# Kernel optimization log

Measured on AMD Instinct MI355X. Metric: run time of the kernel, lower is better.

## Reference

```python
import jax, jax.numpy as jnp
import numpy as np


def setup_inputs() -> dict:
    key = jax.random.key(0)
    k1, k2 = jax.random.split(key)
    B, N, M, D = 8, 4096, 4096, 128
    points1 = jax.random.normal(k1, (B, N, D), dtype=jnp.float32)
    points2 = jax.random.normal(k2, (B, M, D), dtype=jnp.float32)
    return {"points1": points1, "points2": points2}


def reference(points1, points2):
    # sum((x[:, :, None] - y[:, None, :])**2, -1), expressed as a GEMM).
    sq1 = jnp.sum(points1 * points1, axis=-1)              # [B, N]
    sq2 = jnp.sum(points2 * points2, axis=-1)              # [B, M]
    cross = jnp.einsum("bnd,bmd->bnm", points1, points2)   # [B, N, M]
    dist_matrix = sq1[:, :, None] + sq2[:, None, :] - 2.0 * cross
    min_dist1 = jnp.min(dist_matrix, axis=2)               # [B, N]
    min_dist2 = jnp.min(dist_matrix, axis=1)               # [B, M]
    return jnp.mean(min_dist1) + jnp.mean(min_dist2)
```

## Files before the change

### kernel.cpp

```cpp
#include <hip/hip_runtime.h>
#include <hip/hip_bf16.h>


#define BATCH 8
#define NPTS 4096
#define DIM 128

using bf16x8 = __attribute__((ext_vector_type(8))) short;
using f32x4  = __attribute__((ext_vector_type(4))) float;

__global__ void prep_kernel(const float* __restrict__ p1,
                            const float* __restrict__ p2,
                            __hip_bfloat16* __restrict__ b1,
                            __hip_bfloat16* __restrict__ b2,
                            float* __restrict__ s1,
                            float* __restrict__ s2) {
    const int arr = blockIdx.y;
    const float* src = arr ? p2 : p1;
    __hip_bfloat16* dst = arr ? b2 : b1;
    float* sq = arr ? s2 : s1;
    const float scale = arr ? 1.0f : -2.0f;

    const int wid = threadIdx.x >> 6;
    const int l   = threadIdx.x & 63;
    const int p   = blockIdx.x * 4 + wid;
    const float2 v = *reinterpret_cast<const float2*>(src + (size_t)p * DIM + l * 2);
    float s = v.x * v.x + v.y * v.y;
    __hip_bfloat162 h = __float22bfloat162_rn(make_float2(v.x * scale, v.y * scale));
    *reinterpret_cast<__hip_bfloat162*>(dst + (size_t)p * DIM + l * 2) = h;
    #pragma unroll
    for (int off = 1; off < 64; off <<= 1) s += __shfl_xor(s, off);
    if (l == 0) sq[p] = s;
}

__device__ __forceinline__ void stage16(const __hip_bfloat16* g, void* lds) {
    __builtin_amdgcn_global_load_lds(
        (const __attribute__((address_space(1))) void*)g,
        (__attribute__((address_space(3))) void*)lds, 16, 0, 0);
}

__global__ void __launch_bounds__(256, 2)
chamfer_tile_kernel(const __hip_bfloat16* __restrict__ bf1,
                    const __hip_bfloat16* __restrict__ bf2,
                    const float* __restrict__ sq1,
                    const float* __restrict__ sq2,
                    float* __restrict__ min1p,
                    float* __restrict__ min2p) {
    const int nt = blockIdx.x;
    const int mh = blockIdx.y;
    const int b  = blockIdx.z;
    const int tid = threadIdx.x;
    const int wid = tid >> 6;
    const int l   = tid & 63;
    const int l15 = l & 15;
    const int lhi = l >> 4;

    __shared__ __align__(16) unsigned char btile[2][128 * 256];

    const __hip_bfloat16* bf1b = bf1 + (size_t)b * NPTS * DIM;
    const __hip_bfloat16* bf2b = bf2 + (size_t)b * NPTS * DIM;
    const float* sq2b = sq2 + b * NPTS;

    const int n0 = nt * 128 + wid * 32;

    bf16x8 afrag[2][4];
    #pragma unroll
    for (int rt = 0; rt < 2; ++rt)
        #pragma unroll
        for (int ks = 0; ks < 4; ++ks)
            afrag[rt][ks] = *reinterpret_cast<const bf16x8*>(
                bf1b + (n0 + rt * 16 + l15) * DIM + ks * 32 + lhi * 8);

    float sq1v[2][4];
    #pragma unroll
    for (int rt = 0; rt < 2; ++rt)
        #pragma unroll
        for (int j = 0; j < 4; ++j)
            sq1v[rt][j] = sq1[b * NPTS + n0 + rt * 16 + lhi * 4 + j];

    float rmin[2][4];
    #pragma unroll
    for (int rt = 0; rt < 2; ++rt)
        #pragma unroll
        for (int j = 0; j < 4; ++j) rmin[rt][j] = 3.4e38f;

    auto STAGE = [&](int buf, int m0) {
        #pragma unroll
        for (int j = 0; j < 8; ++j) {
            const int c   = j * 256 + wid * 64 + l;
            const int row = c >> 4;
            const int q   = c & 15;
            const __hip_bfloat16* src =
                bf2b + (size_t)(m0 + row) * DIM + (q ^ (row & 7)) * 8;
            stage16(src, &btile[buf][(j * 256 + wid * 64) * 16]);
        }
    };

    int cur = 0;
    STAGE(0, mh * 1024);
    __syncthreads();

    for (int mt = 0; mt < 8; ++mt) {
        const int m0 = mh * 1024 + mt * 128;
        if (mt < 7) STAGE(cur ^ 1, m0 + 128);

        f32x4 acc[2][8];
        #pragma unroll
        for (int rt = 0; rt < 2; ++rt)
            #pragma unroll
            for (int ct = 0; ct < 8; ++ct) acc[rt][ct] = f32x4{0.f, 0.f, 0.f, 0.f};

        #pragma unroll
        for (int ks = 0; ks < 4; ++ks) {
            #pragma unroll
            for (int ct = 0; ct < 8; ++ct) {
                const int brow = ct * 16 + l15;
                const int kbyte = ks * 64 + lhi * 16;
                bf16x8 bfrag = *reinterpret_cast<const bf16x8*>(
                    &btile[cur][brow * 256 + (kbyte ^ ((brow & 7) << 4))]);
                #pragma unroll
                for (int rt = 0; rt < 2; ++rt)
                    acc[rt][ct] = __builtin_amdgcn_mfma_f32_16x16x32_bf16(
                        afrag[rt][ks], bfrag, acc[rt][ct], 0, 0, 0);
            }
        }

        float s2v[8];
        #pragma unroll
        for (int ct = 0; ct < 8; ++ct) s2v[ct] = sq2b[m0 + ct * 16 + l15];

        #pragma unroll
        for (int rt = 0; rt < 2; ++rt)
            #pragma unroll
            for (int j = 0; j < 4; ++j) {
                float r = rmin[rt][j];
                #pragma unroll
                for (int cp = 0; cp < 4; ++cp) {
                    const float t0 = acc[rt][2 * cp][j]     + s2v[2 * cp];
                    const float t1 = acc[rt][2 * cp + 1][j] + s2v[2 * cp + 1];
                    r = fminf(r, fminf(t0, t1));
                }
                rmin[rt][j] = r;
            }

        float cmin[8];
        #pragma unroll
        for (int ct = 0; ct < 8; ++ct) {
            float c = 3.4e38f;
            #pragma unroll
            for (int rt = 0; rt < 2; ++rt)
                #pragma unroll
                for (int jp = 0; jp < 2; ++jp) {
                    const float u0 = sq1v[rt][2 * jp]     + acc[rt][ct][2 * jp];
                    const float u1 = sq1v[rt][2 * jp + 1] + acc[rt][ct][2 * jp + 1];
                    c = fminf(c, fminf(u0, u1));
                }
            cmin[ct] = c;
        }

        #pragma unroll
        for (int ct = 0; ct < 8; ++ct) {
            cmin[ct] = fminf(cmin[ct], __shfl_xor(cmin[ct], 16));
            cmin[ct] = fminf(cmin[ct], __shfl_xor(cmin[ct], 32));
        }
        if (l < 16) {
            float* dst = min2p + ((size_t)b * 128 + nt * 4 + wid) * NPTS + m0;
            #pragma unroll
            for (int ct = 0; ct < 8; ++ct) dst[ct * 16 + l] = cmin[ct];
        }

        __syncthreads();
        cur ^= 1;
    }

    #pragma unroll
    for (int rt = 0; rt < 2; ++rt)
        #pragma unroll
        for (int j = 0; j < 4; ++j) {
            float v = rmin[rt][j];
            v = fminf(v, __shfl_xor(v, 1));
            v = fminf(v, __shfl_xor(v, 2));
            v = fminf(v, __shfl_xor(v, 4));
            v = fminf(v, __shfl_xor(v, 8));
            rmin[rt][j] = v;
        }
    if (l15 == 0) {
        #pragma unroll
        for (int rt = 0; rt < 2; ++rt)
            #pragma unroll
            for (int j = 0; j < 4; ++j)
                min1p[((size_t)b * 4 + mh) * NPTS + n0 + rt * 16 + lhi * 4 + j] =
                    rmin[rt][j];
    }
}

__global__ void finalize_kernel(const float* __restrict__ min1p,
                                const float* __restrict__ min2p,
                                const float* __restrict__ sq1,
                                const float* __restrict__ sq2,
                                float* __restrict__ out) {
    const int tid = threadIdx.x;
    const int gid = blockIdx.x * 256 + tid;
    float sum;

    if (gid < BATCH * NPTS) {
        const int b = gid >> 12, n = gid & (NPTS - 1);
        const float* p = min1p + (size_t)b * 4 * NPTS + n;
        float v = fminf(fminf(p[0], p[NPTS]), fminf(p[2 * NPTS], p[3 * NPTS]));
        sum = (v + sq1[gid]) * (1.0f / (BATCH * NPTS));
    } else {
        const int idx = gid - BATCH * NPTS;
        const int b = idx >> 12, m = idx & (NPTS - 1);
        const float* p = min2p + (size_t)b * 128 * NPTS + m;
        float v0 = 3.4e38f, v1 = 3.4e38f;
        #pragma unroll 4
        for (int j = 0; j < 128; j += 2) {
            v0 = fminf(v0, p[(size_t)j * NPTS]);
            v1 = fminf(v1, p[(size_t)(j + 1) * NPTS]);
        }
        sum = (fminf(v0, v1) + sq2[idx]) * (1.0f / (BATCH * NPTS));
    }

    #pragma unroll
    for (int off = 1; off < 64; off <<= 1) sum += __shfl_xor(sum, off);
    __shared__ float wsum[4];
    if ((tid & 63) == 0) wsum[tid >> 6] = sum;
    __syncthreads();
    if (tid == 0) atomicAdd(out, wsum[0] + wsum[1] + wsum[2] + wsum[3]);
}

extern "C" void kernel_launch(void* const* d_in, const int* in_sizes, int n_in,
                              void* d_out, int out_size, void* d_ws, size_t ws_size,
                              hipStream_t stream) {
    const float* p1 = (const float*)d_in[0];
    const float* p2 = (const float*)d_in[1];
    float* out = (float*)d_out;

    const size_t npts_tot = (size_t)BATCH * NPTS;
    __hip_bfloat16* bf1 = (__hip_bfloat16*)d_ws;
    __hip_bfloat16* bf2 = bf1 + npts_tot * DIM;
    float* sq1   = (float*)(bf2 + npts_tot * DIM);
    float* sq2   = sq1 + npts_tot;
    float* min1p = sq2 + npts_tot;
    float* min2p = min1p + (size_t)BATCH * 4 * NPTS;

    hipMemsetAsync(d_out, 0, sizeof(float), stream);

    prep_kernel<<<dim3(npts_tot / 4, 2), 256, 0, stream>>>(p1, p2, bf1, bf2, sq1, sq2);

    dim3 g2(32, 4, BATCH);
    chamfer_tile_kernel<<<g2, 256, 0, stream>>>(bf1, bf2, sq1, sq2, min1p, min2p);

    finalize_kernel<<<256, 256, 0, stream>>>(min1p, min2p, sq1, sq2, out);
}
```

Measured before the change: 139.6 us.

## Replace partial-min buffers with biased-float atomicMin and shrink M tile to 64

```diff
diff --git a/kernel.cpp b/kernel.cpp
--- a/kernel.cpp
+++ b/kernel.cpp
@@ -5,6 +5,7 @@
 #define BATCH 8
 #define NPTS 4096
 #define DIM 128
+#define FBIAS 16384.0f
 
 using bf16x8 = __attribute__((ext_vector_type(8))) short;
 using f32x4  = __attribute__((ext_vector_type(4))) float;
@@ -44,18 +45,20 @@
                     const __hip_bfloat16* __restrict__ bf2,
                     const float* __restrict__ sq1,
                     const float* __restrict__ sq2,
-                    float* __restrict__ min1p,
-                    float* __restrict__ min2p) {
-    const int nt = blockIdx.x;
-    const int mh = blockIdx.y;
-    const int b  = blockIdx.z;
+                    unsigned int* __restrict__ min1u,
+                    unsigned int* __restrict__ min2u) {
+    const int lin = blockIdx.x;
+    const int b   = lin & 7;
+    const int rest = lin >> 3;
+    const int nt  = rest & 31;
+    const int mh  = rest >> 5;
     const int tid = threadIdx.x;
     const int wid = tid >> 6;
     const int l   = tid & 63;
     const int l15 = l & 15;
     const int lhi = l >> 4;
 
-    __shared__ __align__(16) unsigned char btile[2][128 * 256];
+    __shared__ __align__(16) unsigned char btile[2][64 * 256];
 
     const __hip_bfloat16* bf1b = bf1 + (size_t)b * NPTS * DIM;
     const __hip_bfloat16* bf2b = bf2 + (size_t)b * NPTS * DIM;
@@ -86,7 +89,7 @@
 
     auto STAGE = [&](int buf, int m0) {
         #pragma unroll
-        for (int j = 0; j < 8; ++j) {
+        for (int j = 0; j < 4; ++j) {
             const int c   = j * 256 + wid * 64 + l;
             const int row = c >> 4;
             const int q   = c & 15;
@@ -100,20 +103,20 @@
     STAGE(0, mh * 1024);
     __syncthreads();
 
-    for (int mt = 0; mt < 8; ++mt) {
-        const int m0 = mh * 1024 + mt * 128;
-        if (mt < 7) STAGE(cur ^ 1, m0 + 128);
-
-        f32x4 acc[2][8];
+    for (int mt = 0; mt < 16; ++mt) {
+        const int m0 = mh * 1024 + mt * 64;
+        if (mt < 15) STAGE(cur ^ 1, m0 + 64);
+
+        f32x4 acc[2][4];
         #pragma unroll
         for (int rt = 0; rt < 2; ++rt)
             #pragma unroll
-            for (int ct = 0; ct < 8; ++ct) acc[rt][ct] = f32x4{0.f, 0.f, 0.f, 0.f};
+            for (int ct = 0; ct < 4; ++ct) acc[rt][ct] = f32x4{0.f, 0.f, 0.f, 0.f};
 
         #pragma unroll
         for (int ks = 0; ks < 4; ++ks) {
             #pragma unroll
-            for (int ct = 0; ct < 8; ++ct) {
+            for (int ct = 0; ct < 4; ++ct) {
                 const int brow = ct * 16 + l15;
                 const int kbyte = ks * 64 + lhi * 16;
                 bf16x8 bfrag = *reinterpret_cast<const bf16x8*>(
@@ -125,9 +128,9 @@
             }
         }
 
-        float s2v[8];
-        #pragma unroll
-        for (int ct = 0; ct < 8; ++ct) s2v[ct] = sq2b[m0 + ct * 16 + l15];
+        float s2v[4];
+        #pragma unroll
+        for (int ct = 0; ct < 4; ++ct) s2v[ct] = sq2b[m0 + ct * 16 + l15];
 
         #pragma unroll
         for (int rt = 0; rt < 2; ++rt)
@@ -135,7 +138,7 @@
             for (int j = 0; j < 4; ++j) {
                 float r = rmin[rt][j];
                 #pragma unroll
-                for (int cp = 0; cp < 4; ++cp) {
+                for (int cp = 0; cp < 2; ++cp) {
                     const float t0 = acc[rt][2 * cp][j]     + s2v[2 * cp];
                     const float t1 = acc[rt][2 * cp + 1][j] + s2v[2 * cp + 1];
                     r = fminf(r, fminf(t0, t1));
@@ -143,9 +146,9 @@
                 rmin[rt][j] = r;
             }
 
-        float cmin[8];
-        #pragma unroll
-        for (int ct = 0; ct < 8; ++ct) {
+        float cmin[4];
+        #pragma unroll
+        for (int ct = 0; ct < 4; ++ct) {
             float c = 3.4e38f;
             #pragma unroll
             for (int rt = 0; rt < 2; ++rt)
@@ -159,14 +162,17 @@
         }
 
         #pragma unroll
-        for (int ct = 0; ct < 8; ++ct) {
+        for (int ct = 0; ct < 4; ++ct) {
             cmin[ct] = fminf(cmin[ct], __shfl_xor(cmin[ct], 16));
             cmin[ct] = fminf(cmin[ct], __shfl_xor(cmin[ct], 32));
         }
-        if (l < 16) {
-            float* dst = min2p + ((size_t)b * 128 + nt * 4 + wid) * NPTS + m0;
-            #pragma unroll
-            for (int ct = 0; ct < 8; ++ct) dst[ct * 16 + l] = cmin[ct];
+        {
+            float v = cmin[0];
+            v = (lhi == 1) ? cmin[1] : v;
+            v = (lhi == 2) ? cmin[2] : v;
+            v = (lhi == 3) ? cmin[3] : v;
+            atomicMin(&min2u[(size_t)b * NPTS + m0 + l],
+                      __float_as_uint(v + FBIAS));
         }
 
         __syncthreads();
@@ -189,13 +195,13 @@
         for (int rt = 0; rt < 2; ++rt)
             #pragma unroll
             for (int j = 0; j < 4; ++j)
-                min1p[((size_t)b * 4 + mh) * NPTS + n0 + rt * 16 + lhi * 4 + j] =
-                    rmin[rt][j];
+                atomicMin(&min1u[(size_t)b * NPTS + n0 + rt * 16 + lhi * 4 + j],
+                          __float_as_uint(rmin[rt][j] + FBIAS));
     }
 }
 
-__global__ void finalize_kernel(const float* __restrict__ min1p,
-                                const float* __restrict__ min2p,
+__global__ void finalize_kernel(const unsigned int* __restrict__ min1u,
+                                const unsigned int* __restrict__ min2u,
                                 const float* __restrict__ sq1,
                                 const float* __restrict__ sq2,
                                 float* __restrict__ out) {
@@ -204,21 +210,12 @@
     float sum;
 
     if (gid < BATCH * NPTS) {
-        const int b = gid >> 12, n = gid & (NPTS - 1);
-        const float* p = min1p + (size_t)b * 4 * NPTS + n;
-        float v = fminf(fminf(p[0], p[NPTS]), fminf(p[2 * NPTS], p[3 * NPTS]));
-        sum = (v + sq1[gid]) * (1.0f / (BATCH * NPTS));
+        sum = (__uint_as_float(min1u[gid]) - FBIAS + sq1[gid])
+              * (1.0f / (BATCH * NPTS));
     } else {
         const int idx = gid - BATCH * NPTS;
-        const int b = idx >> 12, m = idx & (NPTS - 1);
-        const float* p = min2p + (size_t)b * 128 * NPTS + m;
-        float v0 = 3.4e38f, v1 = 3.4e38f;
-        #pragma unroll 4
-        for (int j = 0; j < 128; j += 2) {
-            v0 = fminf(v0, p[(size_t)j * NPTS]);
-            v1 = fminf(v1, p[(size_t)(j + 1) * NPTS]);
-        }
-        sum = (fminf(v0, v1) + sq2[idx]) * (1.0f / (BATCH * NPTS));
+        sum = (__uint_as_float(min2u[idx]) - FBIAS + sq2[idx])
+              * (1.0f / (BATCH * NPTS));
     }
 
     #pragma unroll
@@ -239,17 +236,17 @@
     const size_t npts_tot = (size_t)BATCH * NPTS;
     __hip_bfloat16* bf1 = (__hip_bfloat16*)d_ws;
     __hip_bfloat16* bf2 = bf1 + npts_tot * DIM;
-    float* sq1   = (float*)(bf2 + npts_tot * DIM);
-    float* sq2   = sq1 + npts_tot;
-    float* min1p = sq2 + npts_tot;
-    float* min2p = min1p + (size_t)BATCH * 4 * NPTS;
+    float* sq1 = (float*)(bf2 + npts_tot * DIM);
+    float* sq2 = sq1 + npts_tot;
+    unsigned int* min1u = (unsigned int*)(sq2 + npts_tot);
+    unsigned int* min2u = min1u + npts_tot;
 
     hipMemsetAsync(d_out, 0, sizeof(float), stream);
+    hipMemsetAsync(min1u, 0xFF, npts_tot * 2 * sizeof(unsigned int), stream);
 
     prep_kernel<<<dim3(npts_tot / 4, 2), 256, 0, stream>>>(p1, p2, bf1, bf2, sq1, sq2);
 
-    dim3 g2(32, 4, BATCH);
-    chamfer_tile_kernel<<<g2, 256, 0, stream>>>(bf1, bf2, sq1, sq2, min1p, min2p);
-
-    finalize_kernel<<<256, 256, 0, stream>>>(min1p, min2p, sq1, sq2, out);
-}
+    chamfer_tile_kernel<<<1024, 256, 0, stream>>>(bf1, bf2, sq1, sq2, min1u, min2u);
+
+    finalize_kernel<<<256, 256, 0, stream>>>(min1u, min2u, sq1, sq2, out);
+}
```

Result: slower. 163.0 us (+16.8%).
